# Kernel optimization log

Hardware: AMD Instinct MI355X
Metric: run time of the kernel (lower is better)

The kernel has to match this reference:

```python
import jax, jax.numpy as jnp
import numpy as np

T, B, E = 2048, 2, 1024
H = 16
D = E // H


def setup_inputs() -> dict:
    key = jax.random.key(0)
    ks = jax.random.split(key, 7)
    s = 1.0 / np.sqrt(E)
    return {
        "query": jax.random.normal(ks[0], (T, B, E), jnp.float32),
        "key": jax.random.normal(ks[1], (T, B, E), jnp.float32),
        "value": jax.random.normal(ks[2], (T, B, E), jnp.float32),
        "in_proj_weight": jax.random.normal(ks[3], (3 * E, E), jnp.float32) * s,
        "in_proj_bias": jax.random.normal(ks[4], (3 * E,), jnp.float32) * 0.02,
        "out_proj_weight": jax.random.normal(ks[5], (E, E), jnp.float32) * s,
        "out_proj_bias": jax.random.normal(ks[6], (E,), jnp.float32) * 0.02,
    }


def reference(query, key, value, in_proj_weight, in_proj_bias, out_proj_weight, out_proj_bias):
    tgt_len, bsz, embed_dim = query.shape
    src_len = key.shape[0]
    head_dim = embed_dim // H
    # packed in-projection (F.linear: x @ W.T + b)
    w_q, w_k, w_v = jnp.split(in_proj_weight, 3, axis=0)
    b_q, b_k, b_v = jnp.split(in_proj_bias, 3, axis=0)
    q = query @ w_q.T + b_q   # [T, B, E]
    k = key @ w_k.T + b_k     # [S, B, E]
    v = value @ w_v.T + b_v   # [S, B, E]
    # [T,B,E] -> [B,H,T,D]
    q = q.reshape(tgt_len, bsz, H, head_dim).transpose(1, 2, 0, 3)
    k = k.reshape(src_len, bsz, H, head_dim).transpose(1, 2, 0, 3)
    v = v.reshape(src_len, bsz, H, head_dim).transpose(1, 2, 0, 3)
    scale = 1.0 / jnp.sqrt(jnp.asarray(head_dim, q.dtype))
    scores = jnp.einsum("bhtd,bhsd->bhts", q, k) * scale  # [B,H,T,S]
    attn_weights = jax.nn.softmax(scores, axis=-1)
    attn = jnp.einsum("bhts,bhsd->bhtd", attn_weights, v)  # [B,H,T,D]
    # [B,H,T,D] -> [T,B,E]
    attn = attn.transpose(2, 0, 1, 3).reshape(tgt_len, bsz, embed_dim)
    attn_output = attn @ out_proj_weight.T + out_proj_bias  # [T,B,E]
    # averaged attention weights over heads (average_attn_weights=True)
    avg_weights = jnp.sum(attn_weights, axis=1) / H  # [B,T,S]
    return attn_output, avg_weights
```

## Files before the change

kernel.cpp:

```cpp
#include <hip/hip_runtime.h>
#include <hip/hip_bf16.h>

typedef float  f32x2  __attribute__((ext_vector_type(2)));
typedef float  f32x4  __attribute__((ext_vector_type(4)));
typedef float  f32x16 __attribute__((ext_vector_type(16)));
typedef __bf16 bf16x8 __attribute__((ext_vector_type(8)));

#define MFMA16(A,B,C) __builtin_amdgcn_mfma_f32_16x16x32_bf16((A),(B),(C),0,0,0)
#define MFMA32(A,B,C) __builtin_amdgcn_mfma_f32_32x32x16_bf16((A),(B),(C),0,0,0)
#define EXP2(x) __builtin_amdgcn_exp2f(x)
#define LOG2(x) __builtin_amdgcn_logf(x)

static constexpr int Tn = 2048, Bn = 2, En = 1024, Hn = 16, Dn = 64;
static constexpr float kQScale = 0.125f * 1.4426950408889634f;

#define FSWZ(r) (((r) & 7) ^ ((((r) >> 3) & 3) << 1))

static __device__ __forceinline__ unsigned pack2(float a, float b) {
  union { __bf16 h[2]; unsigned u; } un;
  un.h[0] = (__bf16)a; un.h[1] = (__bf16)b;
  return un.u;
}

static __device__ __forceinline__ void gload_lds16(const void* g, void* l) {
  __builtin_amdgcn_global_load_lds(
      (const __attribute__((address_space(1))) void*)g,
      (__attribute__((address_space(3))) void*)l, 16, 0, 0);
}

__global__ __launch_bounds__(256)
void k_cvtw(const float* __restrict__ w3, const float* __restrict__ wo,
            __bf16* __restrict__ w3b, __bf16* __restrict__ wob)
{
  const size_t g = (size_t)blockIdx.x * 256 + threadIdx.x;
  const float* src;
  __bf16* dst;
  size_t off;
  if (g < 393216) { src = w3; dst = w3b; off = g; }
  else            { src = wo; dst = wob; off = g - 393216; }
  const float* p = src + off * 8;
  f32x4 a = *reinterpret_cast<const f32x4*>(p);
  f32x4 b = *reinterpret_cast<const f32x4*>(p + 4);
  bf16x8 o;
  #pragma unroll
  for (int e = 0; e < 4; ++e) { o[e] = (__bf16)a[e]; o[e + 4] = (__bf16)b[e]; }
  *reinterpret_cast<bf16x8*>(dst + off * 8) = o;
}

__global__ __launch_bounds__(256)
void k_qkv(const float* __restrict__ Xq, const float* __restrict__ Xk,
           const float* __restrict__ Xv, const __bf16* __restrict__ W,
           const float* __restrict__ bias,
           __bf16* __restrict__ q_ws, __bf16* __restrict__ k_ws,
           __bf16* __restrict__ v_ws)
{
  __shared__ __align__(16) char a_lds[2][16384];
  __shared__ __align__(16) char b_lds[2][8192];
  const int tid = threadIdx.x;
  const int lane = tid & 63, w = tid >> 6;
  const int wr = w >> 1, wc = w & 1;
  const int ag = lane >> 4, lr = lane & 15;
  const int mBase = blockIdx.x * 128;
  const int oBase = blockIdx.y * 128;
  const int which = blockIdx.y >> 3;
  const float* X = (which == 0) ? Xq : ((which == 1) ? Xk : Xv);
  const __bf16* Wt = W + (size_t)oBase * En;
  __bf16* dst = (which == 0) ? q_ws : ((which == 1) ? k_ws : v_ws);
  const float oscale = (which == 0) ? kQScale : 1.0f;

  const int srow = (w & 1) * 64 + lane;
  const int gw = w >> 1;
  const float* paj[4];
  const __bf16* pbj[2];
  int aD[4], bD[2];
  #pragma unroll
  for (int j = 0; j < 4; ++j) {
    const int g = 2 * j + gw;
    paj[j] = X + (size_t)(mBase + srow) * En + g * 4;
    aD[j] = g * 2048 + (w & 1) * 1024;
  }
  #pragma unroll
  for (int j = 0; j < 2; ++j) {
    const int g = 2 * j + gw;
    pbj[j] = Wt + (size_t)srow * En + g * 8;
    bD[j] = g * 2048 + (w & 1) * 1024;
  }

  f32x4 acc[4][4];
  #pragma unroll
  for (int i = 0; i < 4; ++i)
    #pragma unroll
    for (int j = 0; j < 4; ++j) { f32x4 z = {0.f, 0.f, 0.f, 0.f}; acc[i][j] = z; }

  #pragma unroll
  for (int j = 0; j < 4; ++j) gload_lds16(paj[j], &a_lds[0][aD[j]]);
  #pragma unroll
  for (int j = 0; j < 2; ++j) gload_lds16(pbj[j], &b_lds[0][bD[j]]);
  __syncthreads();

  for (int kt = 0; kt < 32; ++kt) {
    const int cur = kt & 1, nxt = cur ^ 1;
    if (kt + 1 < 32) {
      const int kk = (kt + 1) * 32;
      #pragma unroll
      for (int j = 0; j < 4; ++j) gload_lds16(paj[j] + kk, &a_lds[nxt][aD[j]]);
      #pragma unroll
      for (int j = 0; j < 2; ++j) gload_lds16(pbj[j] + kk, &b_lds[nxt][bD[j]]);
    }
    bf16x8 af[4], bfr[4];
    #pragma unroll
    for (int mb = 0; mb < 4; ++mb) {
      const int row = wr * 64 + mb * 16 + lr;
      f32x4 lo = *(const f32x4*)(&a_lds[cur][(2 * ag) * 2048 + row * 16]);
      f32x4 hi = *(const f32x4*)(&a_lds[cur][(2 * ag + 1) * 2048 + row * 16]);
      bf16x8 v;
      #pragma unroll
      for (int e = 0; e < 4; ++e) { v[e] = (__bf16)lo[e]; v[e + 4] = (__bf16)hi[e]; }
      af[mb] = v;
    }
    #pragma unroll
    for (int nb = 0; nb < 4; ++nb)
      bfr[nb] = *(const bf16x8*)(&b_lds[cur][ag * 2048 + (wc * 64 + nb * 16 + lr) * 16]);
    #pragma unroll
    for (int mb = 0; mb < 4; ++mb)
      #pragma unroll
      for (int nb = 0; nb < 4; ++nb)
        acc[mb][nb] = MFMA16(af[mb], bfr[nb], acc[mb][nb]);
    __syncthreads();
  }

  #pragma unroll
  for (int nb = 0; nb < 4; ++nb) {
    int oG = oBase + wc * 64 + nb * 16 + lr;
    float bv = bias[oG];
    int oS = oG & (En - 1);
    int h = oS >> 6, d = oS & 63;
    #pragma unroll
    for (int mb = 0; mb < 4; ++mb)
      #pragma unroll
      for (int r = 0; r < 4; ++r) {
        int i = mBase + wr * 64 + mb * 16 + ag * 4 + r;
        int t = i >> 1, b2 = i & 1;
        dst[(((size_t)(b2 * Hn + h)) * Tn + t) * Dn + d] =
            (__bf16)((acc[mb][nb][r] + bv) * oscale);
      }
  }
}

__global__ __launch_bounds__(256)
void k_transpose_v(const __bf16* __restrict__ v_ws, __bf16* __restrict__ vt_ws)
{
  __shared__ __bf16 tile[64][72];
  const int bh = blockIdx.x >> 5;
  const int tt = blockIdx.x & 31;
  const int tid = threadIdx.x;
  const __bf16* src = v_ws + ((size_t)bh * Tn + tt * 64) * Dn;
  #pragma unroll
  for (int it = 0; it < 2; ++it) {
    int gi = tid + it * 256;
    int row = gi >> 3, gg = gi & 7;
    *reinterpret_cast<bf16x8*>(&tile[row][gg * 8]) =
        *reinterpret_cast<const bf16x8*>(src + row * Dn + gg * 8);
  }
  __syncthreads();
  __bf16* dst = vt_ws + (size_t)bh * Dn * Tn + tt * 64;
  #pragma unroll
  for (int it = 0; it < 2; ++it) {
    int gi = tid + it * 256;
    int drow = gi >> 3, tg = gi & 7;
    bf16x8 vv;
    #pragma unroll
    for (int e = 0; e < 8; ++e) vv[e] = tile[tg * 8 + e][drow];
    *reinterpret_cast<bf16x8*>(dst + (size_t)drow * Tn + tg * 8) = vv;
  }
}

__global__ __launch_bounds__(256, 2)
void k_flash(const __bf16* __restrict__ q_ws, const __bf16* __restrict__ k_ws,
             const __bf16* __restrict__ vt_ws, __bf16* __restrict__ ctx,
             float* __restrict__ adj_g)
{
  __shared__ __align__(16) char kv_sm[2 * 16384];

  const int tid = threadIdx.x;
  const int lane = tid & 63, w = tid >> 6;
  const int tl = lane & 31, hi = lane >> 5;
  const int bh = blockIdx.x >> 4;
  const int qt = blockIdx.x & 15;
  const int t0w = qt * 128 + w * 32;

  const __bf16* kbase  = k_ws + (size_t)bh * Tn * Dn;
  const __bf16* vtbase = vt_ws + (size_t)bh * Dn * Tn;

  bf16x8 qf[4];
  {
    const __bf16* qrow = q_ws + ((size_t)bh * Tn + t0w + tl) * Dn + hi * 8;
    #pragma unroll
    for (int c = 0; c < 4; ++c)
      qf[c] = *reinterpret_cast<const bf16x8*>(qrow + c * 16);
  }

  union { unsigned u[4]; bf16x8 v; } onu;
  #pragma unroll
  for (int j = 0; j < 4; ++j) onu.u[j] = 0x3F803F80u;
  const bf16x8 kOne = onu.v;

  f32x16 accO0, accO1, accL;
  #pragma unroll
  for (int i = 0; i < 16; ++i) { accO0[i] = 0.f; accO1[i] = 0.f; accL[i] = 0.f; }
  float m_run = -INFINITY;

  const int r0 = tid >> 3, s0 = tid & 7;
  const int ldso = ((s0 ^ FSWZ(r0)) << 4);
  const int ko0 = r0 * 128 + ldso;
  const int ftl = FSWZ(tl);

  bf16x8 rk0 = *(const bf16x8*)(kbase + r0 * 64 + s0 * 8);
  bf16x8 rk1 = *(const bf16x8*)(kbase + (r0 + 32) * 64 + s0 * 8);
  bf16x8 rv0 = *(const bf16x8*)(vtbase + (size_t)r0 * Tn + s0 * 8);
  bf16x8 rv1 = *(const bf16x8*)(vtbase + (size_t)(r0 + 32) * Tn + s0 * 8);
  *(bf16x8*)(kv_sm + ko0) = rk0;
  *(bf16x8*)(kv_sm + ko0 + 4096) = rk1;
  *(bf16x8*)(kv_sm + 8192 + ko0) = rv0;
  *(bf16x8*)(kv_sm + 8192 + ko0 + 4096) = rv1;

  for (int st = 0; st < 32; ++st) {
    __syncthreads();
    const char* cur = kv_sm + (st & 1) * 16384;
    char* nxt = kv_sm + ((st + 1) & 1) * 16384;
    if (st + 1 < 32) {
      const __bf16* kn = kbase + (size_t)(st + 1) * 64 * Dn;
      const __bf16* vn = vtbase + (st + 1) * 64;
      rk0 = *(const bf16x8*)(kn + r0 * 64 + s0 * 8);
      rk1 = *(const bf16x8*)(kn + (r0 + 32) * 64 + s0 * 8);
      rv0 = *(const bf16x8*)(vn + (size_t)r0 * Tn + s0 * 8);
      rv1 = *(const bf16x8*)(vn + (size_t)(r0 + 32) * Tn + s0 * 8);
    }

    f32x16 sc0, sc1;
    #pragma unroll
    for (int i = 0; i < 16; ++i) { sc0[i] = 0.f; sc1[i] = 0.f; }
    const char* kr0 = cur + tl * 128;
    const char* kr1 = cur + (32 + tl) * 128;
    __builtin_amdgcn_s_setprio(1);
    #pragma unroll
    for (int c = 0; c < 4; ++c) {
      const int off = (((2 * c + hi) ^ ftl) << 4);
      sc0 = MFMA32(*(const bf16x8*)(kr0 + off), qf[c], sc0);
      sc1 = MFMA32(*(const bf16x8*)(kr1 + off), qf[c], sc1);
    }
    __builtin_amdgcn_s_setprio(0);

    float mx[8];
    #pragma unroll
    for (int i = 0; i < 8; ++i)
      mx[i] = fmaxf(fmaxf(sc0[i], sc0[i + 8]), fmaxf(sc1[i], sc1[i + 8]));
    float tm = fmaxf(fmaxf(fmaxf(mx[0], mx[1]), fmaxf(mx[2], mx[3])),
                     fmaxf(fmaxf(mx[4], mx[5]), fmaxf(mx[6], mx[7])));
    tm = fmaxf(tm, __shfl_xor(tm, 32, 64));
    if (__any(tm > m_run + 8.0f)) {
      const float mn = fmaxf(m_run, tm);
      const float es = EXP2(m_run - mn);
      m_run = mn;
      #pragma unroll
      for (int q = 0; q < 4; ++q)
        #pragma unroll
        for (int rr = 0; rr < 4; ++rr) {
          const float e = __shfl(es, 8 * q + 4 * hi + rr, 32);
          accO0[q * 4 + rr] *= e;
          accO1[q * 4 + rr] *= e;
          accL[q * 4 + rr] *= e;
        }
    }
    #pragma unroll
    for (int i = 0; i < 16; ++i) {
      sc0[i] = EXP2(sc0[i] - m_run);
      sc1[i] = EXP2(sc1[i] - m_run);
    }

    unsigned wA0[4], wB0[4], wA1[4], wB1[4];
    #pragma unroll
    for (int g = 0; g < 4; ++g) {
      wA0[g] = pack2(sc0[4 * g],     sc0[4 * g + 1]);
      wB0[g] = pack2(sc0[4 * g + 2], sc0[4 * g + 3]);
      wA1[g] = pack2(sc1[4 * g],     sc1[4 * g + 1]);
      wB1[g] = pack2(sc1[4 * g + 2], sc1[4 * g + 3]);
    }
    bf16x8 pa[2][2];
    #pragma unroll
    for (int sb = 0; sb < 2; ++sb) {
      const unsigned* WA = sb ? wA1 : wA0;
      const unsigned* WB = sb ? wB1 : wB0;
      #pragma unroll
      for (int c = 0; c < 2; ++c) {
        unsigned w0 = WA[2 * c], w2 = WA[2 * c + 1];
        unsigned w1 = WB[2 * c], w3 = WB[2 * c + 1];
        asm("v_permlane32_swap_b32 %0, %1" : "+v"(w0), "+v"(w2));
        asm("v_permlane32_swap_b32 %0, %1" : "+v"(w1), "+v"(w3));
        union { unsigned u[4]; bf16x8 v; } uu;
        uu.u[0] = w0; uu.u[1] = w1; uu.u[2] = w2; uu.u[3] = w3;
        pa[sb][c] = uu.v;
      }
    }

    const char* vr0 = cur + 8192 + tl * 128;
    const char* vr1 = cur + 8192 + (32 + tl) * 128;
    __builtin_amdgcn_s_setprio(1);
    #pragma unroll
    for (int sb = 0; sb < 2; ++sb)
      #pragma unroll
      for (int c = 0; c < 2; ++c) {
        const int off = (((sb * 4 + c * 2 + hi) ^ ftl) << 4);
        accO0 = MFMA32(pa[sb][c], *(const bf16x8*)(vr0 + off), accO0);
        accO1 = MFMA32(pa[sb][c], *(const bf16x8*)(vr1 + off), accO1);
        accL  = MFMA32(pa[sb][c], kOne, accL);
      }
    __builtin_amdgcn_s_setprio(0);

    if (st + 1 < 32) {
      *(bf16x8*)(nxt + ko0) = rk0;
      *(bf16x8*)(nxt + ko0 + 4096) = rk1;
      *(bf16x8*)(nxt + 8192 + ko0) = rv0;
      *(bf16x8*)(nxt + 8192 + ko0 + 4096) = rv1;
    }
  }

  const int b2 = bh >> 4, h = bh & 15;
  float adjv[16];
  #pragma unroll
  for (int q = 0; q < 4; ++q)
    #pragma unroll
    for (int rr = 0; rr < 4; ++rr) {
      const int j = q * 4 + rr;
      const float lv = 1.0f / accL[j];
      const int t = t0w + 8 * q + 4 * hi + rr;
      __bf16* cp = ctx + ((size_t)t * Bn + b2) * En + h * 64 + tl;
      cp[0]  = (__bf16)(accO0[j] * lv);
      cp[32] = (__bf16)(accO1[j] * lv);
      const float mrow = __shfl(m_run, 8 * q + 4 * hi + rr, 32);
      adjv[j] = mrow + LOG2(16.0f * accL[j]);
    }
  if (tl == 0) {
    #pragma unroll
    for (int q = 0; q < 4; ++q)
      #pragma unroll
      for (int rr = 0; rr < 4; ++rr) {
        const int t = t0w + 8 * q + 4 * hi + rr;
        adj_g[(size_t)bh * Tn + t] = adjv[q * 4 + rr];
      }
  }
}

__global__ __launch_bounds__(256)
void k_avgw(const __bf16* __restrict__ q_ws, const __bf16* __restrict__ k_ws,
            const float* __restrict__ adj_g, float* __restrict__ avg_out)
{
  __shared__ __align__(16) char q_sm[2][8192];
  __shared__ __align__(16) char k_sm[2][8192];
  __shared__ __align__(16) float adj_sm[16][64];

  const int tid = threadIdx.x;
  const int lane = tid & 63, w = tid >> 6;
  const int tl = lane & 31, hi = lane >> 5;
  const int b2 = blockIdx.x >> 10;
  const int tt = (blockIdx.x >> 5) & 31;
  const int ss = blockIdx.x & 31;
  const int thalf = (w >> 1) * 32, shalf = (w & 1) * 32;

  #pragma unroll
  for (int it = 0; it < 4; ++it) {
    int idx = tid + it * 256;
    int h = idx >> 6, trow = idx & 63;
    adj_sm[h][trow] = adj_g[((size_t)(b2 * Hn + h)) * Tn + tt * 64 + trow];
  }

  const size_t hstride = (size_t)Tn * Dn;
  const __bf16* qb = q_ws + ((size_t)(b2 * Hn) * Tn + tt * 64) * Dn;
  const __bf16* kb = k_ws + ((size_t)(b2 * Hn) * Tn + ss * 64) * Dn;

  const int r0 = tid >> 3, s0 = tid & 7;
  const int ldso = ((s0 ^ FSWZ(r0)) << 4);
  const int ko0 = r0 * 128 + ldso;
  const int ftl = FSWZ(tl);

  bf16x8 rq0 = *(const bf16x8*)(qb + r0 * 64 + s0 * 8);
  bf16x8 rq1 = *(const bf16x8*)(qb + (r0 + 32) * 64 + s0 * 8);
  bf16x8 rk0 = *(const bf16x8*)(kb + r0 * 64 + s0 * 8);
  bf16x8 rk1 = *(const bf16x8*)(kb + (r0 + 32) * 64 + s0 * 8);
  *(bf16x8*)(q_sm[0] + ko0) = rq0;
  *(bf16x8*)(q_sm[0] + ko0 + 4096) = rq1;
  *(bf16x8*)(k_sm[0] + ko0) = rk0;
  *(bf16x8*)(k_sm[0] + ko0 + 4096) = rk1;

  f32x16 avg;
  #pragma unroll
  for (int i = 0; i < 16; ++i) avg[i] = 0.f;

  for (int h = 0; h < Hn; ++h) {
    __syncthreads();
    const char* qc = q_sm[h & 1];
    const char* kc = k_sm[h & 1];
    char* qn = q_sm[(h + 1) & 1];
    char* kn = k_sm[(h + 1) & 1];
    if (h + 1 < Hn) {
      const __bf16* qp = qb + (size_t)(h + 1) * hstride;
      const __bf16* kp2 = kb + (size_t)(h + 1) * hstride;
      rq0 = *(const bf16x8*)(qp + r0 * 64 + s0 * 8);
      rq1 = *(const bf16x8*)(qp + (r0 + 32) * 64 + s0 * 8);
      rk0 = *(const bf16x8*)(kp2 + r0 * 64 + s0 * 8);
      rk1 = *(const bf16x8*)(kp2 + (r0 + 32) * 64 + s0 * 8);
    }

    f32x16 sc;
    #pragma unroll
    for (int i = 0; i < 16; ++i) sc[i] = 0.f;
    const char* qr = qc + (thalf + tl) * 128;
    const char* kr = kc + (shalf + tl) * 128;
    #pragma unroll
    for (int c = 0; c < 4; ++c) {
      const int off = (((2 * c + hi) ^ ftl) << 4);
      sc = MFMA32(*(const bf16x8*)(qr + off), *(const bf16x8*)(kr + off), sc);
    }

    #pragma unroll
    for (int q = 0; q < 4; ++q) {
      f32x4 ad = *(const f32x4*)&adj_sm[h][thalf + 8 * q + 4 * hi];
      #pragma unroll
      for (int r = 0; r < 4; ++r)
        avg[q * 4 + r] += EXP2(sc[q * 4 + r] - ad[r]);
    }

    if (h + 1 < Hn) {
      *(bf16x8*)(qn + ko0) = rq0;
      *(bf16x8*)(qn + ko0 + 4096) = rq1;
      *(bf16x8*)(kn + ko0) = rk0;
      *(bf16x8*)(kn + ko0 + 4096) = rk1;
    }
  }

  #pragma unroll
  for (int q = 0; q < 4; ++q)
    #pragma unroll
    for (int r = 0; r < 4; ++r) {
      int t = tt * 64 + thalf + 8 * q + 4 * hi + r;
      int s = ss * 64 + shalf + tl;
      avg_out[((size_t)(b2 * Tn + t)) * Tn + s] = avg[q * 4 + r];
    }
}

__global__ __launch_bounds__(256)
void k_outproj(const __bf16* __restrict__ ctx, const __bf16* __restrict__ W,
               const float* __restrict__ bias, float* __restrict__ out)
{
  __shared__ __align__(16) char a_lds[2][8192];
  __shared__ __align__(16) char b_lds[2][4096];
  const int tid = threadIdx.x;
  const int lane = tid & 63, w = tid >> 6;
  const int ag = lane >> 4, lr = lane & 15;
  const int mBase = blockIdx.x * 128;
  const int oBase = blockIdx.y * 64;

  const int srow = (w & 1) * 64 + lane;
  const int gw = w >> 1;
  const __bf16* paj[2];
  int aD[2];
  #pragma unroll
  for (int j = 0; j < 2; ++j) {
    const int g = 2 * j + gw;
    paj[j] = ctx + (size_t)(mBase + srow) * En + g * 8;
    aD[j] = g * 2048 + (w & 1) * 1024;
  }
  const __bf16* pb = W + (size_t)(oBase + lane) * En + w * 8;
  const int bDst = w * 1024;

  f32x4 acc[2][4];
  #pragma unroll
  for (int i = 0; i < 2; ++i)
    #pragma unroll
    for (int j = 0; j < 4; ++j) { f32x4 z = {0.f,0.f,0.f,0.f}; acc[i][j] = z; }

  #pragma unroll
  for (int j = 0; j < 2; ++j) gload_lds16(paj[j], &a_lds[0][aD[j]]);
  gload_lds16(pb, &b_lds[0][bDst]);
  __syncthreads();

  for (int kt = 0; kt < 32; ++kt) {
    const int cur = kt & 1, nxt = cur ^ 1;
    if (kt + 1 < 32) {
      const int kk = (kt + 1) * 32;
      #pragma unroll
      for (int j = 0; j < 2; ++j) gload_lds16(paj[j] + kk, &a_lds[nxt][aD[j]]);
      gload_lds16(pb + kk, &b_lds[nxt][bDst]);
    }
    bf16x8 af[2], bfr[4];
    #pragma unroll
    for (int mb = 0; mb < 2; ++mb)
      af[mb] = *(const bf16x8*)(&a_lds[cur][ag * 2048 + (w * 32 + mb * 16 + lr) * 16]);
    #pragma unroll
    for (int nb = 0; nb < 4; ++nb)
      bfr[nb] = *(const bf16x8*)(&b_lds[cur][ag * 1024 + (nb * 16 + lr) * 16]);
    #pragma unroll
    for (int mb = 0; mb < 2; ++mb)
      #pragma unroll
      for (int nb = 0; nb < 4; ++nb)
        acc[mb][nb] = MFMA16(af[mb], bfr[nb], acc[mb][nb]);
    __syncthreads();
  }

  #pragma unroll
  for (int nb = 0; nb < 4; ++nb) {
    int o = oBase + nb * 16 + lr;
    float bv = bias[o];
    #pragma unroll
    for (int mb = 0; mb < 2; ++mb)
      #pragma unroll
      for (int r = 0; r < 4; ++r) {
        int i = mBase + w * 32 + mb * 16 + ag * 4 + r;
        out[(size_t)i * En + o] = acc[mb][nb][r] + bv;
      }
  }
}

extern "C" void kernel_launch(void* const* d_in, const int* in_sizes, int n_in,
                              void* d_out, int out_size, void* d_ws, size_t ws_size,
                              hipStream_t stream)
{
  (void)in_sizes; (void)n_in; (void)out_size; (void)ws_size;
  const float* query = (const float*)d_in[0];
  const float* key   = (const float*)d_in[1];
  const float* value = (const float*)d_in[2];
  const float* in_w  = (const float*)d_in[3];
  const float* in_b  = (const float*)d_in[4];
  const float* out_w = (const float*)d_in[5];
  const float* out_b = (const float*)d_in[6];

  float* attn_out = (float*)d_out;
  float* avg_out  = (float*)d_out + (size_t)Tn * Bn * En;

  char* ws = (char*)d_ws;
  const size_t MB = 1u << 20;
  __bf16* q_ws  = (__bf16*)(ws);
  __bf16* k_ws  = (__bf16*)(ws + 8 * MB);
  __bf16* v_ws  = (__bf16*)(ws + 16 * MB);
  __bf16* vt_ws = (__bf16*)(ws + 24 * MB);
  __bf16* ctx   = (__bf16*)(ws + 32 * MB);
  float*  adj_g = (float*)(ws + 40 * MB);
  __bf16* w3_bf = (__bf16*)(ws + 41 * MB);
  __bf16* wo_bf = (__bf16*)(ws + 47 * MB);

  k_cvtw<<<2048, 256, 0, stream>>>(in_w, out_w, w3_bf, wo_bf);
  k_qkv<<<dim3(32, 24), 256, 0, stream>>>(query, key, value, w3_bf, in_b,
                                          q_ws, k_ws, v_ws);
  k_transpose_v<<<1024, 256, 0, stream>>>(v_ws, vt_ws);
  k_flash<<<512, 256, 0, stream>>>(q_ws, k_ws, vt_ws, ctx, adj_g);
  k_avgw<<<2048, 256, 0, stream>>>(q_ws, k_ws, adj_g, avg_out);
  k_outproj<<<dim3(32, 16), 256, 0, stream>>>(ctx, wo_bf, out_b, attn_out);
}
```

Measured before the change: 217.6 us.

## Fuse V transpose into QKV projection and convert A tile to bf16 before LDS

The separate V-transpose kernel is removed, and the QKV projection kernel now writes V directly in transposed [bh][d][t] layout. The fp32 activation tile is loaded into registers, converted to bf16 and then stored to LDS, which halves A-tile LDS space and drops the per-iteration conversion in the MFMA loop. The LDS swizzle in the flash and avg kernels is simplified to a plain XOR with row&7. This saves one launch plus a V round-trip through memory and reduces LDS traffic. In exchange, the transposed V stores are strided scalar writes, and the A-tile loads go through registers instead of direct-to-LDS loads, which adds register pressure and latency exposure.

```diff
diff --git a/kernel.cpp b/kernel.cpp
--- a/kernel.cpp
+++ b/kernel.cpp
@@ -13,8 +13,6 @@
 
 static constexpr int Tn = 2048, Bn = 2, En = 1024, Hn = 16, Dn = 64;
 static constexpr float kQScale = 0.125f * 1.4426950408889634f;
-
-#define FSWZ(r) (((r) & 7) ^ ((((r) >> 3) & 3) << 1))
 
 static __device__ __forceinline__ unsigned pack2(float a, float b) {
   union { __bf16 h[2]; unsigned u; } un;
@@ -52,9 +50,9 @@
            const float* __restrict__ Xv, const __bf16* __restrict__ W,
            const float* __restrict__ bias,
            __bf16* __restrict__ q_ws, __bf16* __restrict__ k_ws,
-           __bf16* __restrict__ v_ws)
+           __bf16* __restrict__ vt_ws)
 {
-  __shared__ __align__(16) char a_lds[2][16384];
+  __shared__ __align__(16) char a_lds[2][8192];
   __shared__ __align__(16) char b_lds[2][8192];
   const int tid = threadIdx.x;
   const int lane = tid & 63, w = tid >> 6;
@@ -65,26 +63,34 @@
   const int which = blockIdx.y >> 3;
   const float* X = (which == 0) ? Xq : ((which == 1) ? Xk : Xv);
   const __bf16* Wt = W + (size_t)oBase * En;
-  __bf16* dst = (which == 0) ? q_ws : ((which == 1) ? k_ws : v_ws);
   const float oscale = (which == 0) ? kQScale : 1.0f;
 
-  const int srow = (w & 1) * 64 + lane;
-  const int gw = w >> 1;
-  const float* paj[4];
-  const __bf16* pbj[2];
-  int aD[4], bD[2];
-  #pragma unroll
-  for (int j = 0; j < 4; ++j) {
-    const int g = 2 * j + gw;
-    paj[j] = X + (size_t)(mBase + srow) * En + g * 4;
-    aD[j] = g * 2048 + (w & 1) * 1024;
-  }
-  #pragma unroll
-  for (int j = 0; j < 2; ++j) {
-    const int g = 2 * j + gw;
-    pbj[j] = Wt + (size_t)srow * En + g * 8;
-    bD[j] = g * 2048 + (w & 1) * 1024;
-  }
+  const int gA = w;
+  const float* pxa0 = X + (size_t)(mBase + lane) * En + gA * 8;
+  const float* pxa1 = X + (size_t)(mBase + 64 + lane) * En + gA * 8;
+  const __bf16* pb0 = Wt + (size_t)lane * En + gA * 8;
+  const __bf16* pb1 = Wt + (size_t)(64 + lane) * En + gA * 8;
+  const int dA0 = gA * 2048 + lane * 16;
+  const int dA1 = gA * 2048 + 1024 + lane * 16;
+
+  f32x4 a0lo, a0hi, a1lo, a1hi;
+
+#define ALOAD(KK) do {                                                       \
+    a0lo = *(const f32x4*)(pxa0 + (KK));                                     \
+    a0hi = *(const f32x4*)(pxa0 + (KK) + 4);                                 \
+    a1lo = *(const f32x4*)(pxa1 + (KK));                                     \
+    a1hi = *(const f32x4*)(pxa1 + (KK) + 4);                                 \
+  } while (0)
+#define AWRITE(BUF) do {                                                     \
+    bf16x8 v0, v1;                                                           \
+    _Pragma("unroll")                                                        \
+    for (int e = 0; e < 4; ++e) {                                            \
+      v0[e] = (__bf16)a0lo[e]; v0[e + 4] = (__bf16)a0hi[e];                  \
+      v1[e] = (__bf16)a1lo[e]; v1[e + 4] = (__bf16)a1hi[e];                  \
+    }                                                                        \
+    *(bf16x8*)(&a_lds[(BUF)][dA0]) = v0;                                     \
+    *(bf16x8*)(&a_lds[(BUF)][dA1]) = v1;                                     \
+  } while (0)
 
   f32x4 acc[4][4];
   #pragma unroll
@@ -92,32 +98,24 @@
     #pragma unroll
     for (int j = 0; j < 4; ++j) { f32x4 z = {0.f, 0.f, 0.f, 0.f}; acc[i][j] = z; }
 
-  #pragma unroll
-  for (int j = 0; j < 4; ++j) gload_lds16(paj[j], &a_lds[0][aD[j]]);
-  #pragma unroll
-  for (int j = 0; j < 2; ++j) gload_lds16(pbj[j], &b_lds[0][bD[j]]);
+  ALOAD(0);
+  AWRITE(0);
+  gload_lds16(pb0, &b_lds[0][gA * 2048]);
+  gload_lds16(pb1, &b_lds[0][gA * 2048 + 1024]);
   __syncthreads();
 
   for (int kt = 0; kt < 32; ++kt) {
     const int cur = kt & 1, nxt = cur ^ 1;
     if (kt + 1 < 32) {
       const int kk = (kt + 1) * 32;
-      #pragma unroll
-      for (int j = 0; j < 4; ++j) gload_lds16(paj[j] + kk, &a_lds[nxt][aD[j]]);
-      #pragma unroll
-      for (int j = 0; j < 2; ++j) gload_lds16(pbj[j] + kk, &b_lds[nxt][bD[j]]);
+      ALOAD(kk);
+      gload_lds16(pb0 + kk, &b_lds[nxt][gA * 2048]);
+      gload_lds16(pb1 + kk, &b_lds[nxt][gA * 2048 + 1024]);
     }
     bf16x8 af[4], bfr[4];
     #pragma unroll
-    for (int mb = 0; mb < 4; ++mb) {
-      const int row = wr * 64 + mb * 16 + lr;
-      f32x4 lo = *(const f32x4*)(&a_lds[cur][(2 * ag) * 2048 + row * 16]);
-      f32x4 hi = *(const f32x4*)(&a_lds[cur][(2 * ag + 1) * 2048 + row * 16]);
-      bf16x8 v;
-      #pragma unroll
-      for (int e = 0; e < 4; ++e) { v[e] = (__bf16)lo[e]; v[e + 4] = (__bf16)hi[e]; }
-      af[mb] = v;
-    }
+    for (int mb = 0; mb < 4; ++mb)
+      af[mb] = *(const bf16x8*)(&a_lds[cur][ag * 2048 + (wr * 64 + mb * 16 + lr) * 16]);
     #pragma unroll
     for (int nb = 0; nb < 4; ++nb)
       bfr[nb] = *(const bf16x8*)(&b_lds[cur][ag * 2048 + (wc * 64 + nb * 16 + lr) * 16]);
@@ -126,9 +124,13 @@
       #pragma unroll
       for (int nb = 0; nb < 4; ++nb)
         acc[mb][nb] = MFMA16(af[mb], bfr[nb], acc[mb][nb]);
+    if (kt + 1 < 32) AWRITE(nxt);
     __syncthreads();
   }
-
+#undef ALOAD
+#undef AWRITE
+
+  __bf16* dqk = (which == 0) ? q_ws : k_ws;
   #pragma unroll
   for (int nb = 0; nb < 4; ++nb) {
     int oG = oBase + wc * 64 + nb * 16 + lr;
@@ -141,37 +143,12 @@
       for (int r = 0; r < 4; ++r) {
         int i = mBase + wr * 64 + mb * 16 + ag * 4 + r;
         int t = i >> 1, b2 = i & 1;
-        dst[(((size_t)(b2 * Hn + h)) * Tn + t) * Dn + d] =
-            (__bf16)((acc[mb][nb][r] + bv) * oscale);
+        __bf16 val = (__bf16)((acc[mb][nb][r] + bv) * oscale);
+        if (which == 2)
+          vt_ws[(((size_t)(b2 * Hn + h)) * Dn + d) * Tn + t] = val;
+        else
+          dqk[(((size_t)(b2 * Hn + h)) * Tn + t) * Dn + d] = val;
       }
-  }
-}
-
-__global__ __launch_bounds__(256)
-void k_transpose_v(const __bf16* __restrict__ v_ws, __bf16* __restrict__ vt_ws)
-{
-  __shared__ __bf16 tile[64][72];
-  const int bh = blockIdx.x >> 5;
-  const int tt = blockIdx.x & 31;
-  const int tid = threadIdx.x;
-  const __bf16* src = v_ws + ((size_t)bh * Tn + tt * 64) * Dn;
-  #pragma unroll
-  for (int it = 0; it < 2; ++it) {
-    int gi = tid + it * 256;
-    int row = gi >> 3, gg = gi & 7;
-    *reinterpret_cast<bf16x8*>(&tile[row][gg * 8]) =
-        *reinterpret_cast<const bf16x8*>(src + row * Dn + gg * 8);
-  }
-  __syncthreads();
-  __bf16* dst = vt_ws + (size_t)bh * Dn * Tn + tt * 64;
-  #pragma unroll
-  for (int it = 0; it < 2; ++it) {
-    int gi = tid + it * 256;
-    int drow = gi >> 3, tg = gi & 7;
-    bf16x8 vv;
-    #pragma unroll
-    for (int e = 0; e < 8; ++e) vv[e] = tile[tg * 8 + e][drow];
-    *reinterpret_cast<bf16x8*>(dst + (size_t)drow * Tn + tg * 8) = vv;
   }
 }
 
@@ -211,9 +188,8 @@
   float m_run = -INFINITY;
 
   const int r0 = tid >> 3, s0 = tid & 7;
-  const int ldso = ((s0 ^ FSWZ(r0)) << 4);
+  const int ldso = ((s0 ^ (r0 & 7)) << 4);
   const int ko0 = r0 * 128 + ldso;
-  const int ftl = FSWZ(tl);
 
   bf16x8 rk0 = *(const bf16x8*)(kbase + r0 * 64 + s0 * 8);
   bf16x8 rk1 = *(const bf16x8*)(kbase + (r0 + 32) * 64 + s0 * 8);
@@ -245,7 +221,7 @@
     __builtin_amdgcn_s_setprio(1);
     #pragma unroll
     for (int c = 0; c < 4; ++c) {
-      const int off = (((2 * c + hi) ^ ftl) << 4);
+      const int off = (((2 * c + hi) ^ (tl & 7)) << 4);
       sc0 = MFMA32(*(const bf16x8*)(kr0 + off), qf[c], sc0);
       sc1 = MFMA32(*(const bf16x8*)(kr1 + off), qf[c], sc1);
     }
@@ -310,7 +286,7 @@
     for (int sb = 0; sb < 2; ++sb)
       #pragma unroll
       for (int c = 0; c < 2; ++c) {
-        const int off = (((sb * 4 + c * 2 + hi) ^ ftl) << 4);
+        const int off = (((sb * 4 + c * 2 + hi) ^ (tl & 7)) << 4);
         accO0 = MFMA32(pa[sb][c], *(const bf16x8*)(vr0 + off), accO0);
         accO1 = MFMA32(pa[sb][c], *(const bf16x8*)(vr1 + off), accO1);
         accL  = MFMA32(pa[sb][c], kOne, accL);
@@ -379,9 +355,8 @@
   const __bf16* kb = k_ws + ((size_t)(b2 * Hn) * Tn + ss * 64) * Dn;
 
   const int r0 = tid >> 3, s0 = tid & 7;
-  const int ldso = ((s0 ^ FSWZ(r0)) << 4);
+  const int ldso = ((s0 ^ (r0 & 7)) << 4);
   const int ko0 = r0 * 128 + ldso;
-  const int ftl = FSWZ(tl);
 
   bf16x8 rq0 = *(const bf16x8*)(qb + r0 * 64 + s0 * 8);
   bf16x8 rq1 = *(const bf16x8*)(qb + (r0 + 32) * 64 + s0 * 8);
@@ -418,7 +393,7 @@
     const char* kr = kc + (shalf + tl) * 128;
     #pragma unroll
     for (int c = 0; c < 4; ++c) {
-      const int off = (((2 * c + hi) ^ ftl) << 4);
+      const int off = (((2 * c + hi) ^ (tl & 7)) << 4);
       sc = MFMA32(*(const bf16x8*)(qr + off), *(const bf16x8*)(kr + off), sc);
     }
 
@@ -541,17 +516,15 @@
   const size_t MB = 1u << 20;
   __bf16* q_ws  = (__bf16*)(ws);
   __bf16* k_ws  = (__bf16*)(ws + 8 * MB);
-  __bf16* v_ws  = (__bf16*)(ws + 16 * MB);
-  __bf16* vt_ws = (__bf16*)(ws + 24 * MB);
-  __bf16* ctx   = (__bf16*)(ws + 32 * MB);
-  float*  adj_g = (float*)(ws + 40 * MB);
-  __bf16* w3_bf = (__bf16*)(ws + 41 * MB);
-  __bf16* wo_bf = (__bf16*)(ws + 47 * MB);
+  __bf16* vt_ws = (__bf16*)(ws + 16 * MB);
+  __bf16* ctx   = (__bf16*)(ws + 24 * MB);
+  float*  adj_g = (float*)(ws + 32 * MB);
+  __bf16* w3_bf = (__bf16*)(ws + 33 * MB);
+  __bf16* wo_bf = (__bf16*)(ws + 39 * MB);
 
   k_cvtw<<<2048, 256, 0, stream>>>(in_w, out_w, w3_bf, wo_bf);
   k_qkv<<<dim3(32, 24), 256, 0, stream>>>(query, key, value, w3_bf, in_b,
-                                          q_ws, k_ws, v_ws);
-  k_transpose_v<<<1024, 256, 0, stream>>>(v_ws, vt_ws);
+                                          q_ws, k_ws, vt_ws);
   k_flash<<<512, 256, 0, stream>>>(q_ws, k_ws, vt_ws, ctx, adj_g);
   k_avgw<<<2048, 256, 0, stream>>>(q_ws, k_ws, adj_g, avg_out);
   k_outproj<<<dim3(32, 16), 256, 0, stream>>>(ctx, wo_bf, out_b, attn_out);
```

New measurement: 217.1 us. No clear change (-0.2%).
